# Optimization experiments

Measured on AMD Instinct MI355X. Metric: run time of the kernel, lower is better.

## Reference

```python
import jax, jax.numpy as jnp
import numpy as np

TEMPERATURE = 0.1
BASE_TEMPERATURE = 0.07
EPS = 1e-10


def setup_inputs() -> dict:
    key = jax.random.key(0)
    k1, k2 = jax.random.split(key)
    # feats_: [total_classes=64, n_view=128, feat_dim=256] sampled anchor features
    feats_ = jax.random.normal(k1, (64, 128, 256), dtype=jnp.float32)
    # labels_: class id per anchor group (21-class dataset -> repeats across groups)
    labels_ = jax.random.randint(k2, (64,), 0, 21, dtype=jnp.int32)
    return {"feats_": feats_, "labels_": labels_}


def reference(feats_, labels_):
    anchor_num, n_view, d = feats_.shape
    N = anchor_num * n_view
    # torch.cat(torch.unbind(feats_, dim=1), dim=0): view-major flattening
    cf = jnp.transpose(feats_, (1, 0, 2)).reshape(N, d)  # [N, d]
    # labels for the flattened ordering (mask.repeat tiles the [A,A] eq-mask)
    big_labels = jnp.tile(labels_, n_view)  # [N]

    logits = jnp.matmul(cf, cf.T) / TEMPERATURE  # [N, N]
    logits = logits - jax.lax.stop_gradient(jnp.max(logits, axis=1, keepdims=True))

    mask = (big_labels[:, None] == big_labels[None, :]).astype(jnp.float32)
    neg_mask = 1.0 - mask                       # negatives BEFORE removing diagonal
    mask = mask * (1.0 - jnp.eye(N, dtype=jnp.float32))  # positives exclude self

    exp_logits = jnp.exp(logits)
    neg_logits = jnp.sum(exp_logits * neg_mask, axis=1, keepdims=True)  # [N, 1]
    log_prob = logits - jnp.log(exp_logits + neg_logits + EPS)
    mean_log_prob_pos = jnp.sum(mask * log_prob, axis=1) / jnp.sum(mask, axis=1)
    loss = jnp.mean(-(TEMPERATURE / BASE_TEMPERATURE) * mean_log_prob_pos)
    return loss
```

## Files before the change

### kernel.cpp

```cpp
#include <hip/hip_runtime.h>
#include <hip/hip_bf16.h>

#define N_ROWS 8192
#define DIM 256
#define NANCH 64
#define NVIEW 128
#define NSTRIP 4
#define APS 16
#define NPART 8

typedef __attribute__((ext_vector_type(8))) short bf16x8;
typedef __attribute__((ext_vector_type(4))) float f32x4;
typedef __attribute__((ext_vector_type(4))) float float4v;
typedef __attribute__((ext_vector_type(4))) unsigned short ushort4v;

__device__ __forceinline__ unsigned short f2bf(float x) {
  union { float f; unsigned int u; } c; c.f = x;
  unsigned int u = c.u;
  unsigned int r = (u + 0x7fffu + ((u >> 16) & 1u)) >> 16;
  return (unsigned short)r;
}

__device__ __forceinline__ float bf2f(unsigned short b) {
  union { unsigned int u; float f; } c; c.u = ((unsigned int)b) << 16;
  return c.f;
}

__device__ __forceinline__ void gload_lds16(const void* g, void* l) {
  __builtin_amdgcn_global_load_lds(
      (const __attribute__((address_space(1))) unsigned int*)g,
      (__attribute__((address_space(3))) unsigned int*)l, 16, 0, 0);
}

__global__ void cast_diag_kernel(const float4v* __restrict__ in,
                                 ushort4v* __restrict__ out,
                                 float* __restrict__ diag) {
  const int w = threadIdx.x >> 6;
  const int l = threadIdx.x & 63;
  const int row = blockIdx.x * 4 + w;
  const float s = 3.16227766016838f;
  float4v v = in[row * 64 + l];
  ushort4v o;
  o.x = f2bf(v.x * s);
  o.y = f2bf(v.y * s);
  o.z = f2bf(v.z * s);
  o.w = f2bf(v.w * s);
  out[row * 64 + l] = o;
  float c0 = bf2f(o.x), c1 = bf2f(o.y), c2 = bf2f(o.z), c3 = bf2f(o.w);
  float ss = c0 * c0 + c1 * c1 + c2 * c2 + c3 * c3;
#pragma unroll
  for (int st = 1; st < 64; st <<= 1) ss += __shfl_xor(ss, st);
  if (l == 0) diag[row] = ss;
}

__global__ __launch_bounds__(512, 4) void pcl_negsum(
    const unsigned short* __restrict__ Xb, const int* __restrict__ labels,
    const float* __restrict__ diag, float* __restrict__ ns_partial) {
  const int rb = blockIdx.x & 63;
  const int part = blockIdx.x >> 6;
  const int strip = part >> 1;
  const int half = part & 1;
  const int tid = threadIdx.x;
  const int wid = tid >> 6;
  const int lane = tid & 63;
  const int lo = lane & 15;
  const int hi = lane >> 4;
  const int rg = wid >> 1;
  const int cg = wid & 1;

  __shared__ unsigned short buf[2][64 * DIM];
  __shared__ float sns[8][32];
  __shared__ float sdiag[128];
  __shared__ int slab[NANCH];

  if (tid < NANCH) slab[tid] = labels[tid];
  if (tid >= 128 && tid < 256) sdiag[tid - 128] = diag[rb * 128 + tid - 128];
  __syncthreads();
  const int myLab = slab[rb];

  bf16x8 afrag[2][8];
#pragma unroll
  for (int ri = 0; ri < 2; ++ri) {
#pragma unroll
    for (int ks = 0; ks < 8; ++ks) {
      const unsigned short* p =
          Xb + (rb * 128 + rg * 32 + ri * 16 + lo) * DIM + ks * 32 + hi * 8;
      afrag[ri][ks] = *(const bf16x8*)p;
      asm volatile("" : "+v"(afrag[ri][ks]));
    }
  }

  float mreg[8], ns[8];
#pragma unroll
  for (int ri = 0; ri < 2; ++ri)
#pragma unroll
    for (int reg = 0; reg < 4; ++reg) {
      mreg[ri * 4 + reg] = sdiag[rg * 32 + ri * 16 + hi * 4 + reg];
      ns[ri * 4 + reg] = 0.f;
    }

  int srcoff[4];
#pragma unroll
  for (int i = 0; i < 4; ++i) {
    int g = i * 512 + tid;
    int col = g >> 5, ch = g & 31;
    srcoff[i] = col * DIM + ((ch ^ (col & 7)) << 3);
  }
  const int ldsbase = wid * 1024;

  const unsigned short* asrc0 =
      Xb + ((size_t)(strip * APS) * NVIEW + half * 64) * DIM;

#pragma unroll
  for (int i = 0; i < 4; ++i)
    gload_lds16(asrc0 + srcoff[i], (char*)&buf[0][0] + ldsbase + i * 8192);
  __syncthreads();

  const int x8 = lo & 7;
  int cb = 0;
  for (int a = 0; a < APS; ++a) {
    if (a + 1 < APS) {
      const unsigned short* src = asrc0 + (size_t)(a + 1) * NVIEW * DIM;
#pragma unroll
      for (int i = 0; i < 4; ++i)
        gload_lds16(src + srcoff[i], (char*)&buf[cb ^ 1][0] + ldsbase + i * 8192);
    }

    const bool isneg = (slab[strip * APS + a] != myLab);
    const char* bufc = (const char*)&buf[cb][0];
    f32x4 acc[2][2];
#pragma unroll
    for (int ri = 0; ri < 2; ++ri)
#pragma unroll
      for (int ci = 0; ci < 2; ++ci)
        acc[ri][ci] = (f32x4){0.f, 0.f, 0.f, 0.f};

#pragma unroll
    for (int ks = 0; ks < 8; ++ks) {
      const int sw = ((ks * 4 + hi) ^ x8) << 4;
      bf16x8 b0 = *(const bf16x8*)(bufc + (cg * 32 + lo) * 512 + sw);
      bf16x8 b1 = *(const bf16x8*)(bufc + (cg * 32 + 16 + lo) * 512 + sw);
      acc[0][0] = __builtin_amdgcn_mfma_f32_16x16x32_bf16(afrag[0][ks], b0, acc[0][0], 0, 0, 0);
      acc[0][1] = __builtin_amdgcn_mfma_f32_16x16x32_bf16(afrag[0][ks], b1, acc[0][1], 0, 0, 0);
      acc[1][0] = __builtin_amdgcn_mfma_f32_16x16x32_bf16(afrag[1][ks], b0, acc[1][0], 0, 0, 0);
      acc[1][1] = __builtin_amdgcn_mfma_f32_16x16x32_bf16(afrag[1][ks], b1, acc[1][1], 0, 0, 0);
    }

    if (isneg) {
#pragma unroll
      for (int ri = 0; ri < 2; ++ri)
#pragma unroll
        for (int reg = 0; reg < 4; ++reg) {
          const int t = ri * 4 + reg;
          float v0 = acc[ri][0][reg];
          float v1 = acc[ri][1][reg];
          if (__builtin_expect(fmaxf(v0, v1) > mreg[t] - 40.f, 0))
            ns[t] += __expf(v0 - mreg[t]) + __expf(v1 - mreg[t]);
        }
    }
    __syncthreads();
    cb ^= 1;
  }

#pragma unroll
  for (int t = 0; t < 8; ++t) {
#pragma unroll
    for (int st = 1; st < 16; st <<= 1) ns[t] += __shfl_xor(ns[t], st);
  }
  if (lo == 0) {
#pragma unroll
    for (int ri = 0; ri < 2; ++ri)
#pragma unroll
      for (int reg = 0; reg < 4; ++reg)
        sns[wid][ri * 16 + hi * 4 + reg] = ns[ri * 4 + reg];
  }
  __syncthreads();
  if (tid < 128) {
    const int rg2 = tid >> 5, r32 = tid & 31;
    float s = sns[rg2 * 2 + 0][r32] + sns[rg2 * 2 + 1][r32];
    ns_partial[part * N_ROWS + rb * 128 + tid] = s;
  }
}

__global__ __launch_bounds__(1024, 4) void pcl_pos(
    const unsigned short* __restrict__ Xb, const int* __restrict__ labels,
    const float* __restrict__ diag, const float* __restrict__ ns_partial,
    float* __restrict__ partials) {
  const int blk = blockIdx.x;
  const int r0 = blk * 32;
  const int tid = threadIdx.x;
  const int wid = tid >> 6;
  const int lane = tid & 63;
  const int lo = lane & 15;
  const int hi = lane >> 4;
  const int cq = wid & 3;
  const int bq = wid >> 2;

  __shared__ int slab[NANCH];
  __shared__ float sred[16][32];
  __shared__ float smf[32];
  __shared__ float snsf[32];
  __shared__ int poslist[NANCH];
  __shared__ int scnt;

  if (tid < NANCH) slab[tid] = labels[tid];
  if (tid >= 64 && tid < 96) {
    int r = tid - 64;
    smf[r] = diag[r0 + r];
    float s = 0.f;
#pragma unroll
    for (int p = 0; p < NPART; ++p) s += ns_partial[p * N_ROWS + r0 + r];
    snsf[r] = s;
  }
  if (tid == 0) {
    int La0 = labels[blk >> 2];
    int c = 0;
    for (int b = 0; b < NANCH; ++b)
      if (labels[b] == La0) poslist[c++] = b;
    scnt = c;
  }
  __syncthreads();

  bf16x8 afrag[2][8];
#pragma unroll
  for (int ri = 0; ri < 2; ++ri) {
#pragma unroll
    for (int ks = 0; ks < 8; ++ks) {
      const unsigned short* p = Xb + (r0 + ri * 16 + lo) * DIM + ks * 32 + hi * 8;
      afrag[ri][ks] = *(const bf16x8*)p;
      asm volatile("" : "+v"(afrag[ri][ks]));
    }
  }

  const int cnt = scnt;
  float pos[8];
#pragma unroll
  for (int t = 0; t < 8; ++t) pos[t] = 0.f;

  for (int p = bq; p < cnt; p += 4) {
    const int b = poslist[p];
    const int c0 = b * NVIEW + cq * 32;
    f32x4 acc[2][2];
#pragma unroll
    for (int ri = 0; ri < 2; ++ri)
#pragma unroll
      for (int ci = 0; ci < 2; ++ci)
        acc[ri][ci] = (f32x4){0.f, 0.f, 0.f, 0.f};

#pragma unroll
    for (int ks = 0; ks < 8; ++ks) {
      bf16x8 b0 = *(const bf16x8*)(Xb + (c0 + lo) * DIM + ks * 32 + hi * 8);
      bf16x8 b1 = *(const bf16x8*)(Xb + (c0 + 16 + lo) * DIM + ks * 32 + hi * 8);
      acc[0][0] = __builtin_amdgcn_mfma_f32_16x16x32_bf16(afrag[0][ks], b0, acc[0][0], 0, 0, 0);
      acc[0][1] = __builtin_amdgcn_mfma_f32_16x16x32_bf16(afrag[0][ks], b1, acc[0][1], 0, 0, 0);
      acc[1][0] = __builtin_amdgcn_mfma_f32_16x16x32_bf16(afrag[1][ks], b0, acc[1][0], 0, 0, 0);
      acc[1][1] = __builtin_amdgcn_mfma_f32_16x16x32_bf16(afrag[1][ks], b1, acc[1][1], 0, 0, 0);
    }

#pragma unroll
    for (int ri = 0; ri < 2; ++ri) {
#pragma unroll
      for (int ci = 0; ci < 2; ++ci) {
#pragma unroll
        for (int reg = 0; reg < 4; ++reg) {
          const int t = ri * 4 + reg;
          const int row = ri * 16 + hi * 4 + reg;
          int grow = r0 + row;
          int gcol = c0 + ci * 16 + lo;
          if (grow != gcol) {
            float d = acc[ri][ci][reg] - smf[row];
            pos[t] += d - __logf(__expf(d) + snsf[row] + 1e-10f);
          }
        }
      }
    }
  }

#pragma unroll
  for (int t = 0; t < 8; ++t) {
#pragma unroll
    for (int st = 1; st < 16; st <<= 1) pos[t] += __shfl_xor(pos[t], st);
  }
  if (lo == 0) {
#pragma unroll
    for (int ri = 0; ri < 2; ++ri)
#pragma unroll
      for (int reg = 0; reg < 4; ++reg)
        sred[wid][ri * 16 + hi * 4 + reg] = pos[ri * 4 + reg];
  }
  __syncthreads();

  const float poscnt = (float)(cnt * NVIEW - 1);
  if (tid < 32) {
    float P = 0.f;
#pragma unroll
    for (int w = 0; w < 16; ++w) P += sred[w][tid];
    smf[tid] = P / poscnt;
  }
  __syncthreads();
  if (tid == 0) {
    float s = 0.f;
    for (int r = 0; r < 32; ++r) s += smf[r];
    partials[blk] = s;
  }
}

__global__ void final_reduce(const float* __restrict__ partials, float* __restrict__ out) {
  __shared__ float s[256];
  int t = threadIdx.x;
  s[t] = partials[t];
  __syncthreads();
  for (int st = 128; st > 0; st >>= 1) {
    if (t < st) s[t] += s[t + st];
    __syncthreads();
  }
  if (t == 0) out[0] = -(0.1f / 0.07f) * s[0] / (float)N_ROWS;
}

extern "C" void kernel_launch(void* const* d_in, const int* in_sizes, int n_in,
                              void* d_out, int out_size, void* d_ws, size_t ws_size,
                              hipStream_t stream) {
  const float* feats = (const float*)d_in[0];
  const int* labels = (const int*)d_in[1];
  float* out = (float*)d_out;

  char* base = (char*)d_ws;
  unsigned short* Xb = (unsigned short*)d_ws;
  float* diag = (float*)(base + (size_t)N_ROWS * DIM * 2);
  float* ns_partial = (float*)(base + (size_t)N_ROWS * DIM * 2 + N_ROWS * 4);
  float* partials = (float*)(base + (size_t)N_ROWS * DIM * 2 + N_ROWS * 4 +
                             NPART * N_ROWS * 4);

  cast_diag_kernel<<<N_ROWS / 4, 256, 0, stream>>>((const float4v*)feats,
                                                   (ushort4v*)Xb, diag);
  pcl_negsum<<<NANCH * NPART, 512, 0, stream>>>(Xb, labels, diag, ns_partial);
  pcl_pos<<<N_ROWS / 32, 1024, 0, stream>>>(Xb, labels, diag, ns_partial, partials);
  final_reduce<<<1, 256, 0, stream>>>(partials, out);
}
```

Before: 77.37 us.

## Switch negsum to 32x32x16 MFMA with new LDS layout and wave-level skip; shrink pos blocks

Reworks the negative-sum kernel so each wave uses one 32x32x16 bf16 MFMA per k-step instead of four 16x16x32 MFMAs, with a new non-swizzled LDS layout that matches the larger fragment. The exp work is gated by a wave-wide any() against a per-wave minimum threshold, so most negative tiles skip the exponential entirely. The positive kernel is cut from 1024 to 512 threads per block, with each wave covering more positive anchors. Risks include LDS bank conflicts from dropping the swizzle, and lower parallelism in the positive kernel.

```diff
diff --git a/kernel.cpp b/kernel.cpp
--- a/kernel.cpp
+++ b/kernel.cpp
@@ -5,12 +5,12 @@
 #define DIM 256
 #define NANCH 64
 #define NVIEW 128
-#define NSTRIP 4
 #define APS 16
 #define NPART 8
 
 typedef __attribute__((ext_vector_type(8))) short bf16x8;
 typedef __attribute__((ext_vector_type(4))) float f32x4;
+typedef __attribute__((ext_vector_type(16))) float f32x16;
 typedef __attribute__((ext_vector_type(4))) float float4v;
 typedef __attribute__((ext_vector_type(4))) unsigned short ushort4v;
 
@@ -63,8 +63,8 @@
   const int tid = threadIdx.x;
   const int wid = tid >> 6;
   const int lane = tid & 63;
-  const int lo = lane & 15;
-  const int hi = lane >> 4;
+  const int l31 = lane & 31;
+  const int khalf = lane >> 5;
   const int rg = wid >> 1;
   const int cg = wid & 1;
 
@@ -78,35 +78,33 @@
   __syncthreads();
   const int myLab = slab[rb];
 
-  bf16x8 afrag[2][8];
-#pragma unroll
-  for (int ri = 0; ri < 2; ++ri) {
-#pragma unroll
-    for (int ks = 0; ks < 8; ++ks) {
-      const unsigned short* p =
-          Xb + (rb * 128 + rg * 32 + ri * 16 + lo) * DIM + ks * 32 + hi * 8;
-      afrag[ri][ks] = *(const bf16x8*)p;
-      asm volatile("" : "+v"(afrag[ri][ks]));
-    }
-  }
-
-  float mreg[8], ns[8];
-#pragma unroll
-  for (int ri = 0; ri < 2; ++ri)
-#pragma unroll
-    for (int reg = 0; reg < 4; ++reg) {
-      mreg[ri * 4 + reg] = sdiag[rg * 32 + ri * 16 + hi * 4 + reg];
-      ns[ri * 4 + reg] = 0.f;
-    }
+  bf16x8 afrag[16];
+#pragma unroll
+  for (int ks = 0; ks < 16; ++ks) {
+    const unsigned short* p =
+        Xb + (size_t)(rb * 128 + rg * 32 + l31) * DIM + ks * 16 + khalf * 8;
+    afrag[ks] = *(const bf16x8*)p;
+    asm volatile("" : "+v"(afrag[ks]));
+  }
+
+  float thr;
+  {
+    float d = sdiag[rg * 32 + l31];
+#pragma unroll
+    for (int st = 1; st < 32; st <<= 1) d = fminf(d, __shfl_xor(d, st));
+    thr = d - 40.f;
+  }
+
+  float ns[16];
+#pragma unroll
+  for (int r = 0; r < 16; ++r) ns[r] = 0.f;
 
   int srcoff[4];
 #pragma unroll
-  for (int i = 0; i < 4; ++i) {
-    int g = i * 512 + tid;
-    int col = g >> 5, ch = g & 31;
-    srcoff[i] = col * DIM + ((ch ^ (col & 7)) << 3);
-  }
+  for (int i = 0; i < 4; ++i) srcoff[i] = lane * DIM + (i * 8 + wid) * 8;
   const int ldsbase = wid * 1024;
+
+  const int boff = khalf * 1024 + cg * 512 + l31 * 16;
 
   const unsigned short* asrc0 =
       Xb + ((size_t)(strip * APS) * NVIEW + half * 64) * DIM;
@@ -116,7 +114,6 @@
     gload_lds16(asrc0 + srcoff[i], (char*)&buf[0][0] + ldsbase + i * 8192);
   __syncthreads();
 
-  const int x8 = lo & 7;
   int cb = 0;
   for (int a = 0; a < APS; ++a) {
     if (a + 1 < APS) {
@@ -126,63 +123,53 @@
         gload_lds16(src + srcoff[i], (char*)&buf[cb ^ 1][0] + ldsbase + i * 8192);
     }
 
-    const bool isneg = (slab[strip * APS + a] != myLab);
     const char* bufc = (const char*)&buf[cb][0];
-    f32x4 acc[2][2];
-#pragma unroll
-    for (int ri = 0; ri < 2; ++ri)
-#pragma unroll
-      for (int ci = 0; ci < 2; ++ci)
-        acc[ri][ci] = (f32x4){0.f, 0.f, 0.f, 0.f};
-
-#pragma unroll
-    for (int ks = 0; ks < 8; ++ks) {
-      const int sw = ((ks * 4 + hi) ^ x8) << 4;
-      bf16x8 b0 = *(const bf16x8*)(bufc + (cg * 32 + lo) * 512 + sw);
-      bf16x8 b1 = *(const bf16x8*)(bufc + (cg * 32 + 16 + lo) * 512 + sw);
-      acc[0][0] = __builtin_amdgcn_mfma_f32_16x16x32_bf16(afrag[0][ks], b0, acc[0][0], 0, 0, 0);
-      acc[0][1] = __builtin_amdgcn_mfma_f32_16x16x32_bf16(afrag[0][ks], b1, acc[0][1], 0, 0, 0);
-      acc[1][0] = __builtin_amdgcn_mfma_f32_16x16x32_bf16(afrag[1][ks], b0, acc[1][0], 0, 0, 0);
-      acc[1][1] = __builtin_amdgcn_mfma_f32_16x16x32_bf16(afrag[1][ks], b1, acc[1][1], 0, 0, 0);
-    }
-
-    if (isneg) {
-#pragma unroll
-      for (int ri = 0; ri < 2; ++ri)
-#pragma unroll
-        for (int reg = 0; reg < 4; ++reg) {
-          const int t = ri * 4 + reg;
-          float v0 = acc[ri][0][reg];
-          float v1 = acc[ri][1][reg];
-          if (__builtin_expect(fmaxf(v0, v1) > mreg[t] - 40.f, 0))
-            ns[t] += __expf(v0 - mreg[t]) + __expf(v1 - mreg[t]);
+    f32x16 acc = {};
+#pragma unroll
+    for (int ks = 0; ks < 16; ++ks) {
+      bf16x8 bfr = *(const bf16x8*)(bufc + ks * 2048 + boff);
+      acc = __builtin_amdgcn_mfma_f32_32x32x16_bf16(afrag[ks], bfr, acc, 0, 0, 0);
+    }
+
+    if (slab[strip * APS + a] != myLab) {
+      float vmax = acc[0];
+#pragma unroll
+      for (int r = 1; r < 16; ++r) vmax = fmaxf(vmax, acc[r]);
+      if (__builtin_expect(__any(vmax > thr), 0)) {
+#pragma unroll
+        for (int r = 0; r < 16; ++r) {
+          const int rr = (r & 3) + 8 * (r >> 2) + 4 * khalf;
+          float mr = sdiag[rg * 32 + rr];
+          float v = acc[r];
+          if (v > mr - 40.f) ns[r] += __expf(v - mr);
         }
+      }
     }
     __syncthreads();
     cb ^= 1;
   }
 
 #pragma unroll
-  for (int t = 0; t < 8; ++t) {
-#pragma unroll
-    for (int st = 1; st < 16; st <<= 1) ns[t] += __shfl_xor(ns[t], st);
-  }
-  if (lo == 0) {
-#pragma unroll
-    for (int ri = 0; ri < 2; ++ri)
-#pragma unroll
-      for (int reg = 0; reg < 4; ++reg)
-        sns[wid][ri * 16 + hi * 4 + reg] = ns[ri * 4 + reg];
+  for (int r = 0; r < 16; ++r) {
+#pragma unroll
+    for (int st = 1; st < 32; st <<= 1) ns[r] += __shfl_xor(ns[r], st);
+  }
+  if (l31 == 0) {
+#pragma unroll
+    for (int r = 0; r < 16; ++r) {
+      const int rr = (r & 3) + 8 * (r >> 2) + 4 * khalf;
+      sns[wid][rr] = ns[r];
+    }
   }
   __syncthreads();
   if (tid < 128) {
-    const int rg2 = tid >> 5, r32 = tid & 31;
-    float s = sns[rg2 * 2 + 0][r32] + sns[rg2 * 2 + 1][r32];
-    ns_partial[part * N_ROWS + rb * 128 + tid] = s;
-  }
-}
-
-__global__ __launch_bounds__(1024, 4) void pcl_pos(
+    const int rg2 = tid >> 5, rr = tid & 31;
+    ns_partial[part * N_ROWS + rb * 128 + tid] =
+        sns[rg2 * 2 + 0][rr] + sns[rg2 * 2 + 1][rr];
+  }
+}
+
+__global__ __launch_bounds__(512, 4) void pcl_pos(
     const unsigned short* __restrict__ Xb, const int* __restrict__ labels,
     const float* __restrict__ diag, const float* __restrict__ ns_partial,
     float* __restrict__ partials) {
@@ -197,7 +184,7 @@
   const int bq = wid >> 2;
 
   __shared__ int slab[NANCH];
-  __shared__ float sred[16][32];
+  __shared__ float sred[8][32];
   __shared__ float smf[32];
   __shared__ float snsf[32];
   __shared__ int poslist[NANCH];
@@ -237,7 +224,7 @@
 #pragma unroll
   for (int t = 0; t < 8; ++t) pos[t] = 0.f;
 
-  for (int p = bq; p < cnt; p += 4) {
+  for (int p = bq; p < cnt; p += 2) {
     const int b = poslist[p];
     const int c0 = b * NVIEW + cq * 32;
     f32x4 acc[2][2];
@@ -294,7 +281,7 @@
   if (tid < 32) {
     float P = 0.f;
 #pragma unroll
-    for (int w = 0; w < 16; ++w) P += sred[w][tid];
+    for (int w = 0; w < 8; ++w) P += sred[w][tid];
     smf[tid] = P / poscnt;
   }
   __syncthreads();
@@ -334,6 +321,6 @@
   cast_diag_kernel<<<N_ROWS / 4, 256, 0, stream>>>((const float4v*)feats,
                                                    (ushort4v*)Xb, diag);
   pcl_negsum<<<NANCH * NPART, 512, 0, stream>>>(Xb, labels, diag, ns_partial);
-  pcl_pos<<<N_ROWS / 32, 1024, 0, stream>>>(Xb, labels, diag, ns_partial, partials);
+  pcl_pos<<<N_ROWS / 32, 512, 0, stream>>>(Xb, labels, diag, ns_partial, partials);
   final_reduce<<<1, 256, 0, stream>>>(partials, out);
 }
```

Result: slower. 83.52 us (+8.0%).
